# Kernel optimization log

Hardware: AMD Instinct MI355X
Metric: run time of the kernel (lower is better)

## Reference

```python
import jax, jax.numpy as jnp
import numpy as np

H = 16
N_TASKS, N_DATA, N_DEV = 400_000, 200_000, 8


def _edges(key, n_src, n_dst, e):
    k1, k2 = jax.random.split(key)
    src = jax.random.randint(k1, (e,), 0, n_src)
    dst = jax.random.randint(k2, (e,), 0, n_dst)
    return jnp.stack([src, dst]).astype(jnp.int64)


def setup_inputs() -> dict:
    key = jax.random.key(0)
    ks = jax.random.split(key, 16)
    inp = {
        "x_tasks": jax.random.normal(ks[0], (N_TASKS, 12), jnp.float32),
        "x_data": jax.random.normal(ks[1], (N_DATA, 5), jnp.float32),
        "x_devices": jax.random.normal(ks[2], (N_DEV, 12), jnp.float32),
        "ei_data_tasks": _edges(ks[3], N_DATA, N_TASKS, 1_600_000),
        "ei_tasks_data": _edges(ks[4], N_TASKS, N_DATA, 1_600_000),
        "ei_tasks_devices": _edges(ks[5], N_TASKS, N_DEV, 400_000),
        "ei_devices_tasks": _edges(ks[6], N_DEV, N_TASKS, 400_000),
        "ei_data_devices": _edges(ks[7], N_DATA, N_DEV, 200_000),
        "ei_devices_data": _edges(ks[8], N_DEV, N_DATA, 200_000),
        "ei_tt_to": _edges(ks[9], N_TASKS, N_TASKS, 800_000),
        "ei_tt_from": _edges(ks[10], N_TASKS, N_TASKS, 800_000),
        # stacked GraphConv weights, grouped by input dim
        # W_rel5:  [0]=data->tasks, [1]=data->devices
        "W_rel5": jax.random.normal(ks[11], (2, 5, H), jnp.float32) * 0.3,
        # W_rel12: [0]=tasks->data,[1]=tasks->devices,[2]=devices->tasks,[3]=devices->data,[4]=tt_to,[5]=tt_from
        "W_rel12": jax.random.normal(ks[12], (6, 12, H), jnp.float32) * 0.2,
        # b_rel order: dt_t, t_d, t_dev, dev_t, d_dev, dev_d, tt_to, tt_from
        "b_rel": jax.random.normal(ks[13], (8, H), jnp.float32) * 0.1,
        # W_root5: [0]=tasks->data (dst data), [1]=devices->data
        "W_root5": jax.random.normal(ks[14], (2, 5, H), jnp.float32) * 0.3,
        # W_root12: [0]=data->tasks,[1]=tasks->devices,[2]=devices->tasks,[3]=data->devices,[4]=tt_to,[5]=tt_from
        "W_root12": jax.random.normal(ks[15], (6, 12, H), jnp.float32) * 0.2,
        # LayerNorm params: [0]=tasks, [1]=data, [2]=devices
        "ln_gamma": jnp.ones((3, H), jnp.float32),
        "ln_beta": jnp.zeros((3, H), jnp.float32),
    }
    return inp


def _graph_conv(x_src, x_dst, ei, W_rel, b_rel, W_root):
    # PyG GraphConv(aggr='add'): lin_rel(scatter_add(x_src[src] -> dst)) + lin_root(x_dst)
    agg = jax.ops.segment_sum(x_src[ei[0]], ei[1], num_segments=x_dst.shape[0])
    return agg @ W_rel + b_rel + x_dst @ W_root


def _layer_norm(x, gamma, beta, eps=1e-5):
    mu = jnp.mean(x, axis=-1, keepdims=True)
    var = jnp.mean(jnp.square(x - mu), axis=-1, keepdims=True)
    return (x - mu) * jax.lax.rsqrt(var + eps) * gamma + beta


def reference(x_tasks, x_data, x_devices,
              ei_data_tasks, ei_tasks_data, ei_tasks_devices, ei_devices_tasks,
              ei_data_devices, ei_devices_data, ei_tt_to, ei_tt_from,
              W_rel5, W_rel12, b_rel, W_root5, W_root12, ln_gamma, ln_beta):
    # HeteroConv(aggr='sum'): sum relation outputs per destination node type
    tasks = (
        _graph_conv(x_data, x_tasks, ei_data_tasks, W_rel5[0], b_rel[0], W_root12[0])
        + _graph_conv(x_devices, x_tasks, ei_devices_tasks, W_rel12[2], b_rel[3], W_root12[2])
        + _graph_conv(x_tasks, x_tasks, ei_tt_to, W_rel12[4], b_rel[6], W_root12[4])
        + _graph_conv(x_tasks, x_tasks, ei_tt_from, W_rel12[5], b_rel[7], W_root12[5])
    )
    data = (
        _graph_conv(x_tasks, x_data, ei_tasks_data, W_rel12[0], b_rel[1], W_root5[0])
        + _graph_conv(x_devices, x_data, ei_devices_data, W_rel12[3], b_rel[5], W_root5[1])
    )
    devices = (
        _graph_conv(x_tasks, x_devices, ei_tasks_devices, W_rel12[1], b_rel[2], W_root12[1])
        + _graph_conv(x_data, x_devices, ei_data_devices, W_rel5[1], b_rel[4], W_root12[3])
    )
    slope = 0.01
    tasks = jax.nn.leaky_relu(_layer_norm(tasks, ln_gamma[0], ln_beta[0]), slope)
    data = jax.nn.leaky_relu(_layer_norm(data, ln_gamma[1], ln_beta[1]), slope)
    devices = jax.nn.leaky_relu(_layer_norm(devices, ln_gamma[2], ln_beta[2]), slope)
    return tasks, data, devices
```

## Files before the change

kernel.cpp:

```cpp
#include <hip/hip_runtime.h>

#define LRELU(v) ((v) >= 0.0f ? (v) : 0.01f * (v))
#define EPB 8192
#define SHIFT_T 7
#define SHIFT_D 8
#define MAXB 3200

struct PartDesc {
    const int* src; const int* dst;
    unsigned int* part; int* cursor;
    int E, B, cap, shift, chunk0;
};
struct PartArgs { PartDesc r[6]; };

__global__ __launch_bounds__(256)
void partition_all_k(PartArgs a)
{
    __shared__ int hist[MAXB];
    __shared__ int base[MAXB];
    const int bid = blockIdx.x;
    int ri = 0;
    #pragma unroll
    for (int k = 1; k < 6; ++k) if (bid >= a.r[k].chunk0) ri = k;
    const PartDesc d = a.r[ri];
    const int t = threadIdx.x;
    const int e0 = (bid - d.chunk0) * EPB;
    const int e1 = min(d.E, e0 + EPB);
    const int B = d.B, sh = d.shift;
    const unsigned mask = (1u << sh) - 1u;

    for (int i = t; i < B; i += 256) hist[i] = 0;
    __syncthreads();
    for (int e = e0 + t; e < e1; e += 256)
        atomicAdd(&hist[d.dst[e] >> sh], 1);
    __syncthreads();
    for (int i = t; i < B; i += 256) {
        int h = hist[i];
        base[i] = h ? atomicAdd(&d.cursor[i], h) : 0;
        hist[i] = 0;
    }
    __syncthreads();
    for (int e = e0 + t; e < e1; e += 256) {
        int dd = d.dst[e];
        int b = dd >> sh;
        int r = atomicAdd(&hist[b], 1) + base[b];
        if (r < d.cap)
            d.part[(size_t)b * d.cap + r] =
                ((unsigned)d.src[e] << sh) | ((unsigned)dd & mask);
    }
}

template<int F>
__device__ __forceinline__ void loadrow(const float* __restrict__ x, unsigned s, float* v) {
    const float* p = x + (size_t)s * F;
    #pragma unroll
    for (int f = 0; f < F; ++f) v[f] = p[f];
}
template<>
__device__ __forceinline__ void loadrow<12>(const float* __restrict__ x, unsigned s, float* v) {
    const float4* p = (const float4*)(x + (size_t)s * 12);
    float4 a = p[0], b = p[1], c = p[2];
    v[0]=a.x; v[1]=a.y; v[2]=a.z; v[3]=a.w;
    v[4]=b.x; v[5]=b.y; v[6]=b.z; v[7]=b.w;
    v[8]=c.x; v[9]=c.y; v[10]=c.z; v[11]=c.w;
}
template<int F>
__device__ __forceinline__ void addrow(float* a, const float* v) {
    #pragma unroll
    for (int f = 0; f < F; ++f) atomicAdd(a + f, v[f]);
}

template<int F, int STRIDE, int BASE, int SHIFT>
__device__ __forceinline__
void agg_rel(const unsigned* __restrict__ p, int cnt, const float* __restrict__ x,
             float* acc, int t)
{
    constexpr unsigned MASK = (1u << SHIFT) - 1u;
    int i = 2 * t;
    for (; i + 1 < cnt; i += 512) {
        uint2 e = *(const uint2*)(p + i);
        float v0[F], v1[F];
        loadrow<F>(x, e.x >> SHIFT, v0);
        loadrow<F>(x, e.y >> SHIFT, v1);
        addrow<F>(acc + (e.x & MASK) * STRIDE + BASE, v0);
        addrow<F>(acc + (e.y & MASK) * STRIDE + BASE, v1);
    }
    if (i < cnt) {
        unsigned e = p[i];
        float v[F];
        loadrow<F>(x, e >> SHIFT, v);
        addrow<F>(acc + (e & MASK) * STRIDE + BASE, v);
    }
}

template<int NF>
__device__ __forceinline__
void dot_ln_store(const float* __restrict__ f, const float* __restrict__ sW,
                  const float* __restrict__ sb, const float* __restrict__ sg,
                  const float* __restrict__ sbt, float* __restrict__ op)
{
    float o[16];
    #pragma unroll
    for (int k = 0; k < 16; ++k) o[k] = sb[k];
    const float4* w4 = (const float4*)sW;
    #pragma unroll
    for (int j = 0; j < NF; ++j) {
        const float fj = f[j];
        float4 w0 = w4[j*4+0], w1 = w4[j*4+1], w2 = w4[j*4+2], w3 = w4[j*4+3];
        o[0] =fmaf(fj,w0.x,o[0]);  o[1] =fmaf(fj,w0.y,o[1]);
        o[2] =fmaf(fj,w0.z,o[2]);  o[3] =fmaf(fj,w0.w,o[3]);
        o[4] =fmaf(fj,w1.x,o[4]);  o[5] =fmaf(fj,w1.y,o[5]);
        o[6] =fmaf(fj,w1.z,o[6]);  o[7] =fmaf(fj,w1.w,o[7]);
        o[8] =fmaf(fj,w2.x,o[8]);  o[9] =fmaf(fj,w2.y,o[9]);
        o[10]=fmaf(fj,w2.z,o[10]); o[11]=fmaf(fj,w2.w,o[11]);
        o[12]=fmaf(fj,w3.x,o[12]); o[13]=fmaf(fj,w3.y,o[13]);
        o[14]=fmaf(fj,w3.z,o[14]); o[15]=fmaf(fj,w3.w,o[15]);
    }
    float mu = 0.0f;
    #pragma unroll
    for (int k = 0; k < 16; ++k) mu += o[k];
    mu *= 0.0625f;
    float var = 0.0f;
    #pragma unroll
    for (int k = 0; k < 16; ++k) { float d = o[k] - mu; var = fmaf(d, d, var); }
    var *= 0.0625f;
    const float r = rsqrtf(var + 1e-5f);
    #pragma unroll
    for (int k = 0; k < 16; ++k) {
        float v = (o[k] - mu) * r * sg[k] + sbt[k];
        op[k] = LRELU(v);
    }
}

struct FinArgs {
    const unsigned *p_dt, *p_devt, *p_to, *p_from, *p_td, *p_devd;
    const int *c_dt, *c_devt, *c_to, *c_from, *c_td, *c_devd;
    int cap_dt, cap_devt, cap_to, cap_from, cap_td, cap_devd;
    const float *x_tasks, *x_data, *x_dev;
    const float *W_rel5, *W_rel12, *b_rel, *W_root5, *W_root12, *ln_g, *ln_b;
    float *out_tasks, *out_data;
    int NT, ND, Bt;
};

__global__ __launch_bounds__(256, 4)
void agg_finalize_k(FinArgs A)
{
    __shared__ __align__(16) float lds[6912];
    const int t = threadIdx.x;

    if ((int)blockIdx.x < A.Bt) {
        float* sW  = lds;
        float* sb  = lds + 848;
        float* sg  = lds + 864;
        float* sbt = lds + 880;
        float* acc = lds + 896;
        const int b  = blockIdx.x;
        const int n0 = b << SHIFT_T;
        const int nn = min(128, A.NT - n0);
        for (int i = t; i < 80; i += 256) sW[i] = A.W_rel5[i];
        for (int i = t; i < 192; i += 256) {
            sW[80  + i] = A.W_rel12[384 + i];
            sW[272 + i] = A.W_rel12[768 + i];
            sW[464 + i] = A.W_rel12[960 + i];
            sW[656 + i] = A.W_root12[i] + A.W_root12[384 + i]
                        + A.W_root12[768 + i] + A.W_root12[960 + i];
        }
        if (t < 16) {
            sb[t]  = A.b_rel[t] + A.b_rel[48 + t] + A.b_rel[96 + t] + A.b_rel[112 + t];
            sg[t]  = A.ln_g[t];
            sbt[t] = A.ln_b[t];
        }
        for (int i = t; i < 128 * 41; i += 256) acc[i] = 0.0f;
        __syncthreads();

        agg_rel<5, 41, 0, SHIFT_T>(A.p_dt   + (size_t)b * A.cap_dt,   min(A.c_dt[b],   A.cap_dt),   A.x_data,  acc, t);
        agg_rel<12,41, 5, SHIFT_T>(A.p_devt + (size_t)b * A.cap_devt, min(A.c_devt[b], A.cap_devt), A.x_dev,   acc, t);
        agg_rel<12,41,17, SHIFT_T>(A.p_to   + (size_t)b * A.cap_to,   min(A.c_to[b],   A.cap_to),   A.x_tasks, acc, t);
        agg_rel<12,41,29, SHIFT_T>(A.p_from + (size_t)b * A.cap_from, min(A.c_from[b], A.cap_from), A.x_tasks, acc, t);
        __syncthreads();

        if (t < nn) {
            float f[53];
            #pragma unroll
            for (int j = 0; j < 41; ++j) f[j] = acc[t * 41 + j];
            const float* xr = A.x_tasks + (size_t)(n0 + t) * 12;
            #pragma unroll
            for (int j = 0; j < 12; ++j) f[41 + j] = xr[j];
            dot_ln_store<53>(f, sW, sb, sg, sbt, A.out_tasks + (size_t)(n0 + t) * 16);
        }
    } else {
        float* sW  = lds;
        float* sb  = lds + 464;
        float* sg  = lds + 480;
        float* sbt = lds + 496;
        float* acc = lds + 512;
        const int b  = blockIdx.x - A.Bt;
        const int n0 = b << SHIFT_D;
        const int nn = min(256, A.ND - n0);
        for (int i = t; i < 192; i += 256) {
            sW[i]       = A.W_rel12[i];
            sW[192 + i] = A.W_rel12[576 + i];
        }
        for (int i = t; i < 80; i += 256)
            sW[384 + i] = A.W_root5[i] + A.W_root5[80 + i];
        if (t < 16) {
            sb[t]  = A.b_rel[16 + t] + A.b_rel[80 + t];
            sg[t]  = A.ln_g[16 + t];
            sbt[t] = A.ln_b[16 + t];
        }
        for (int i = t; i < 256 * 25; i += 256) acc[i] = 0.0f;
        __syncthreads();

        agg_rel<12,25, 0, SHIFT_D>(A.p_td   + (size_t)b * A.cap_td,   min(A.c_td[b],   A.cap_td),   A.x_tasks, acc, t);
        agg_rel<12,25,12, SHIFT_D>(A.p_devd + (size_t)b * A.cap_devd, min(A.c_devd[b], A.cap_devd), A.x_dev,   acc, t);
        __syncthreads();

        if (t < nn) {
            float f[29];
            #pragma unroll
            for (int j = 0; j < 24; ++j) f[j] = acc[t * 25 + j];
            const float* xr = A.x_data + (size_t)(n0 + t) * 5;
            #pragma unroll
            for (int j = 0; j < 5; ++j) f[24 + j] = xr[j];
            dot_ln_store<29>(f, sW, sb, sg, sbt, A.out_data + (size_t)(n0 + t) * 16);
        }
    }
}

template<int F>
__global__ __launch_bounds__(256)
void scatter_dev_k(const float* __restrict__ x, const int* __restrict__ src,
                   const int* __restrict__ dst, int E, float* __restrict__ agg)
{
    __shared__ float s_agg[8 * F];
    for (int i = threadIdx.x; i < 8 * F; i += 256) s_agg[i] = 0.0f;
    __syncthreads();

    float acc[8 * F];
    #pragma unroll
    for (int i = 0; i < 8 * F; ++i) acc[i] = 0.0f;

    const int stride = gridDim.x * blockDim.x;
    for (int e = blockIdx.x * blockDim.x + threadIdx.x; e < E; e += stride) {
        int s = src[e];
        int d = dst[e];
        float xr[F];
        loadrow<F>(x, (unsigned)s, xr);
        #pragma unroll
        for (int dd = 0; dd < 8; ++dd) {
            bool m = (d == dd);
            #pragma unroll
            for (int f = 0; f < F; ++f)
                acc[dd * F + f] += m ? xr[f] : 0.0f;
        }
    }

    const int lane = threadIdx.x & 63;
    #pragma unroll
    for (int i = 0; i < 8 * F; ++i) {
        float v = acc[i];
        #pragma unroll
        for (int off = 32; off; off >>= 1) v += __shfl_down(v, off);
        if (lane == 0) atomicAdd(&s_agg[i], v);
    }
    __syncthreads();
    if (threadIdx.x < 8 * F) atomicAdd(&agg[threadIdx.x], s_agg[threadIdx.x]);
}

__global__ void finalize_dev_k(const float* __restrict__ aggT, const float* __restrict__ aggD,
                               const float* __restrict__ x,
                               const float* __restrict__ W_rel12, const float* __restrict__ W_rel5,
                               const float* __restrict__ b_rel, const float* __restrict__ W_root12,
                               const float* __restrict__ ln_g, const float* __restrict__ ln_b,
                               float* __restrict__ out, int N)
{
    int i = threadIdx.x;
    if (i >= N) return;
    float acc[16];
    #pragma unroll
    for (int k = 0; k < 16; ++k) acc[k] = b_rel[32 + k] + b_rel[64 + k];
    #pragma unroll
    for (int j = 0; j < 12; ++j) {
        float fj = aggT[i * 12 + j];
        #pragma unroll
        for (int k = 0; k < 16; ++k) acc[k] = fmaf(fj, W_rel12[192 + j * 16 + k], acc[k]);
    }
    #pragma unroll
    for (int j = 0; j < 5; ++j) {
        float fj = aggD[i * 5 + j];
        #pragma unroll
        for (int k = 0; k < 16; ++k) acc[k] = fmaf(fj, W_rel5[80 + j * 16 + k], acc[k]);
    }
    #pragma unroll
    for (int j = 0; j < 12; ++j) {
        float fj = x[i * 12 + j];
        #pragma unroll
        for (int k = 0; k < 16; ++k)
            acc[k] = fmaf(fj, W_root12[192 + j * 16 + k] + W_root12[576 + j * 16 + k], acc[k]);
    }
    float mu = 0.0f;
    #pragma unroll
    for (int k = 0; k < 16; ++k) mu += acc[k];
    mu *= 0.0625f;
    float var = 0.0f;
    #pragma unroll
    for (int k = 0; k < 16; ++k) { float d = acc[k] - mu; var = fmaf(d, d, var); }
    var *= 0.0625f;
    const float r = rsqrtf(var + 1e-5f);
    #pragma unroll
    for (int k = 0; k < 16; ++k) {
        float v = (acc[k] - mu) * r * ln_g[32 + k] + ln_b[32 + k];
        out[i * 16 + k] = LRELU(v);
    }
}

extern "C" void kernel_launch(void* const* d_in, const int* in_sizes, int n_in,
                              void* d_out, int out_size, void* d_ws, size_t ws_size,
                              hipStream_t stream)
{
    const float* x_tasks = (const float*)d_in[0];
    const float* x_data  = (const float*)d_in[1];
    const float* x_dev   = (const float*)d_in[2];
    const int* ei_dt    = (const int*)d_in[3];
    const int* ei_td    = (const int*)d_in[4];
    const int* ei_tdev  = (const int*)d_in[5];
    const int* ei_devt  = (const int*)d_in[6];
    const int* ei_ddev  = (const int*)d_in[7];
    const int* ei_devd  = (const int*)d_in[8];
    const int* ei_to    = (const int*)d_in[9];
    const int* ei_from  = (const int*)d_in[10];
    const float* W_rel5   = (const float*)d_in[11];
    const float* W_rel12  = (const float*)d_in[12];
    const float* b_rel    = (const float*)d_in[13];
    const float* W_root5  = (const float*)d_in[14];
    const float* W_root12 = (const float*)d_in[15];
    const float* ln_g     = (const float*)d_in[16];
    const float* ln_b     = (const float*)d_in[17];

    const int NT   = in_sizes[0] / 12;
    const int ND   = in_sizes[1] / 5;
    const int NDEV = in_sizes[2] / 12;
    const int E_dt   = in_sizes[3]  / 2;
    const int E_td   = in_sizes[4]  / 2;
    const int E_tdev = in_sizes[5]  / 2;
    const int E_devt = in_sizes[6]  / 2;
    const int E_ddev = in_sizes[7]  / 2;
    const int E_devd = in_sizes[8]  / 2;
    const int E_to   = in_sizes[9]  / 2;
    const int E_from = in_sizes[10] / 2;

    const int B_t = (NT + 127) / 128;
    const int B_d = (ND + 255) / 256;

    auto capf = [](int E, int B) {
        int mean = E / B + 1;
        int c = mean + 256 + mean / 8;
        return (c + 1) & ~1;
    };
    const int cap_dt   = capf(E_dt,   B_t);
    const int cap_devt = capf(E_devt, B_t);
    const int cap_to   = capf(E_to,   B_t);
    const int cap_from = capf(E_from, B_t);
    const int cap_td   = capf(E_td,   B_d);
    const int cap_devd = capf(E_devd, B_d);

    float* ws = (float*)d_ws;
    size_t o = 0;
    int* c_dt   = (int*)(ws + o); o += MAXB;
    int* c_devt = (int*)(ws + o); o += MAXB;
    int* c_to   = (int*)(ws + o); o += MAXB;
    int* c_from = (int*)(ws + o); o += MAXB;
    int* c_td   = (int*)(ws + o); o += 800;
    int* c_devd = (int*)(ws + o); o += 800;
    float* aggT_dev = ws + o; o += 96;
    float* aggD_dev = ws + o; o += 48;
    const size_t zero_bytes = o * sizeof(float);
    o = (o + 1) & ~(size_t)1;
    unsigned* p_dt   = (unsigned*)(ws + o); o += (size_t)B_t * cap_dt;
    unsigned* p_devt = (unsigned*)(ws + o); o += (size_t)B_t * cap_devt;
    unsigned* p_to   = (unsigned*)(ws + o); o += (size_t)B_t * cap_to;
    unsigned* p_from = (unsigned*)(ws + o); o += (size_t)B_t * cap_from;
    unsigned* p_td   = (unsigned*)(ws + o); o += (size_t)B_d * cap_td;
    unsigned* p_devd = (unsigned*)(ws + o); o += (size_t)B_d * cap_devd;

    hipMemsetAsync(d_ws, 0, zero_bytes, stream);

    auto nc = [](int e) { return (e + EPB - 1) / EPB; };
    PartArgs pa;
    int ch = 0;
    pa.r[0] = { ei_dt,   ei_dt   + E_dt,   p_dt,   c_dt,   E_dt,   B_t, cap_dt,   SHIFT_T, ch }; ch += nc(E_dt);
    pa.r[1] = { ei_devt, ei_devt + E_devt, p_devt, c_devt, E_devt, B_t, cap_devt, SHIFT_T, ch }; ch += nc(E_devt);
    pa.r[2] = { ei_to,   ei_to   + E_to,   p_to,   c_to,   E_to,   B_t, cap_to,   SHIFT_T, ch }; ch += nc(E_to);
    pa.r[3] = { ei_from, ei_from + E_from, p_from, c_from, E_from, B_t, cap_from, SHIFT_T, ch }; ch += nc(E_from);
    pa.r[4] = { ei_td,   ei_td   + E_td,   p_td,   c_td,   E_td,   B_d, cap_td,   SHIFT_D, ch }; ch += nc(E_td);
    pa.r[5] = { ei_devd, ei_devd + E_devd, p_devd, c_devd, E_devd, B_d, cap_devd, SHIFT_D, ch }; ch += nc(E_devd);

    partition_all_k<<<ch, 256, 0, stream>>>(pa);

    scatter_dev_k<12><<<256, 256, 0, stream>>>(x_tasks, ei_tdev, ei_tdev + E_tdev, E_tdev, aggT_dev);
    scatter_dev_k<5> <<<128, 256, 0, stream>>>(x_data,  ei_ddev, ei_ddev + E_ddev, E_ddev, aggD_dev);

    float* out_tasks = (float*)d_out;
    float* out_data  = out_tasks + (size_t)NT * 16;
    float* out_dev   = out_data  + (size_t)ND * 16;

    FinArgs fa;
    fa.p_dt = p_dt; fa.p_devt = p_devt; fa.p_to = p_to; fa.p_from = p_from;
    fa.p_td = p_td; fa.p_devd = p_devd;
    fa.c_dt = c_dt; fa.c_devt = c_devt; fa.c_to = c_to; fa.c_from = c_from;
    fa.c_td = c_td; fa.c_devd = c_devd;
    fa.cap_dt = cap_dt; fa.cap_devt = cap_devt; fa.cap_to = cap_to;
    fa.cap_from = cap_from; fa.cap_td = cap_td; fa.cap_devd = cap_devd;
    fa.x_tasks = x_tasks; fa.x_data = x_data; fa.x_dev = x_dev;
    fa.W_rel5 = W_rel5; fa.W_rel12 = W_rel12; fa.b_rel = b_rel;
    fa.W_root5 = W_root5; fa.W_root12 = W_root12; fa.ln_g = ln_g; fa.ln_b = ln_b;
    fa.out_tasks = out_tasks; fa.out_data = out_data;
    fa.NT = NT; fa.ND = ND; fa.Bt = B_t;

    agg_finalize_k<<<B_t + B_d, 256, 0, stream>>>(fa);

    finalize_dev_k<<<1, 64, 0, stream>>>(
        aggT_dev, aggD_dev, x_dev,
        W_rel12, W_rel5, b_rel, W_root12, ln_g, ln_b, out_dev, NDEV);
}
```

Before: 646.9 us.

## Gather node features from fp16 copies and merge prep kernels into one launch

Adds fp16 padded copies of task and data features, built inside a single merged prep kernel that also runs the edge partitioning and the device-destination scatters. The aggregation now gathers source rows from these half-precision copies, 32 bytes per task row instead of 48, and processes four edges per thread per iteration to expose more memory-level parallelism. The device scatter switches from per-thread masked register accumulation to shared-memory atomics. Intent is to cut gather bandwidth and launch count, at the cost of an extra conversion pass and reduced input precision in the aggregates.

```diff
diff --git a/kernel.cpp b/kernel.cpp
--- a/kernel.cpp
+++ b/kernel.cpp
@@ -1,4 +1,5 @@
 #include <hip/hip_runtime.h>
+#include <hip/hip_fp16.h>
 
 #define LRELU(v) ((v) >= 0.0f ? (v) : 0.01f * (v))
 #define EPB 8192
@@ -11,44 +12,17 @@
     unsigned int* part; int* cursor;
     int E, B, cap, shift, chunk0;
 };
-struct PartArgs { PartDesc r[6]; };
-
-__global__ __launch_bounds__(256)
-void partition_all_k(PartArgs a)
-{
-    __shared__ int hist[MAXB];
-    __shared__ int base[MAXB];
-    const int bid = blockIdx.x;
-    int ri = 0;
-    #pragma unroll
-    for (int k = 1; k < 6; ++k) if (bid >= a.r[k].chunk0) ri = k;
-    const PartDesc d = a.r[ri];
-    const int t = threadIdx.x;
-    const int e0 = (bid - d.chunk0) * EPB;
-    const int e1 = min(d.E, e0 + EPB);
-    const int B = d.B, sh = d.shift;
-    const unsigned mask = (1u << sh) - 1u;
-
-    for (int i = t; i < B; i += 256) hist[i] = 0;
-    __syncthreads();
-    for (int e = e0 + t; e < e1; e += 256)
-        atomicAdd(&hist[d.dst[e] >> sh], 1);
-    __syncthreads();
-    for (int i = t; i < B; i += 256) {
-        int h = hist[i];
-        base[i] = h ? atomicAdd(&d.cursor[i], h) : 0;
-        hist[i] = 0;
-    }
-    __syncthreads();
-    for (int e = e0 + t; e < e1; e += 256) {
-        int dd = d.dst[e];
-        int b = dd >> sh;
-        int r = atomicAdd(&hist[b], 1) + base[b];
-        if (r < d.cap)
-            d.part[(size_t)b * d.cap + r] =
-                ((unsigned)d.src[e] << sh) | ((unsigned)dd & mask);
-    }
-}
+
+struct PrepArgs {
+    PartDesc r[6];
+    int part_end;
+    const int *tdev_e; int E_tdev; int sd12_b0, sd12_nb;
+    const int *ddev_e; int E_ddev; int sd5_b0, sd5_nb;
+    const float *x_tasks, *x_data, *x_dev;
+    float *aggT_dev, *aggD_dev;
+    __half *h_tasks; int NT; int ct_b0;
+    __half *h_data;  int ND; int cd_b0;
+};
 
 template<int F>
 __device__ __forceinline__ void loadrow(const float* __restrict__ x, unsigned s, float* v) {
@@ -64,31 +38,161 @@
     v[4]=b.x; v[5]=b.y; v[6]=b.z; v[7]=b.w;
     v[8]=c.x; v[9]=c.y; v[10]=c.z; v[11]=c.w;
 }
+
+template<int F>
+__device__ void scatter_dev_body(const float* __restrict__ x, const int* __restrict__ src,
+                                 const int* __restrict__ dst, int E,
+                                 float* __restrict__ agg, float* s_agg,
+                                 int bl, int nb, int t)
+{
+    for (int i = t; i < 8 * F; i += 256) s_agg[i] = 0.0f;
+    __syncthreads();
+    const int stride = nb * 256;
+    for (int e = bl * 256 + t; e < E; e += stride) {
+        float v[F];
+        loadrow<F>(x, (unsigned)src[e], v);
+        int d = dst[e];
+        #pragma unroll
+        for (int f = 0; f < F; ++f) atomicAdd(&s_agg[d * F + f], v[f]);
+    }
+    __syncthreads();
+    if (t < 8 * F) atomicAdd(&agg[t], s_agg[t]);
+}
+
+__global__ __launch_bounds__(256)
+void prep_k(PrepArgs A)
+{
+    __shared__ int shmem[2 * MAXB];
+    const int bid = blockIdx.x;
+    const int t = threadIdx.x;
+
+    if (bid < A.part_end) {
+        int* hist = shmem;
+        int* base = shmem + MAXB;
+        int ri = 0;
+        #pragma unroll
+        for (int k = 1; k < 6; ++k) if (bid >= A.r[k].chunk0) ri = k;
+        const PartDesc d = A.r[ri];
+        const int e0 = (bid - d.chunk0) * EPB;
+        const int e1 = min(d.E, e0 + EPB);
+        const int B = d.B, sh = d.shift;
+        const unsigned mask = (1u << sh) - 1u;
+
+        for (int i = t; i < B; i += 256) hist[i] = 0;
+        __syncthreads();
+        for (int e = e0 + t; e < e1; e += 256)
+            atomicAdd(&hist[d.dst[e] >> sh], 1);
+        __syncthreads();
+        for (int i = t; i < B; i += 256) {
+            int h = hist[i];
+            base[i] = h ? atomicAdd(&d.cursor[i], h) : 0;
+            hist[i] = 0;
+        }
+        __syncthreads();
+        for (int e = e0 + t; e < e1; e += 256) {
+            int dd = d.dst[e];
+            int b = dd >> sh;
+            int r = atomicAdd(&hist[b], 1) + base[b];
+            if (r < d.cap)
+                d.part[(size_t)b * d.cap + r] =
+                    ((unsigned)d.src[e] << sh) | ((unsigned)dd & mask);
+        }
+    } else if (bid < A.sd5_b0) {
+        scatter_dev_body<12>(A.x_tasks, A.tdev_e, A.tdev_e + A.E_tdev, A.E_tdev,
+                             A.aggT_dev, (float*)shmem, bid - A.sd12_b0, A.sd12_nb, t);
+    } else if (bid < A.ct_b0) {
+        scatter_dev_body<5>(A.x_data, A.ddev_e, A.ddev_e + A.E_ddev, A.E_ddev,
+                            A.aggD_dev, (float*)shmem, bid - A.sd5_b0, A.sd5_nb, t);
+    } else if (bid < A.cd_b0) {
+        int row = (bid - A.ct_b0) * 256 + t;
+        if (row < A.NT) {
+            const float* xr = A.x_tasks + (size_t)row * 12;
+            __half h[16];
+            #pragma unroll
+            for (int j = 0; j < 12; ++j) h[j] = __float2half(xr[j]);
+            #pragma unroll
+            for (int j = 12; j < 16; ++j) h[j] = __half(0.0f);
+            uint4* dst = (uint4*)(A.h_tasks + (size_t)row * 16);
+            dst[0] = *(const uint4*)h;
+            dst[1] = *(const uint4*)(h + 8);
+        }
+    } else {
+        int row = (bid - A.cd_b0) * 256 + t;
+        if (row < A.ND) {
+            const float* xr = A.x_data + (size_t)row * 5;
+            __half h[8];
+            #pragma unroll
+            for (int j = 0; j < 5; ++j) h[j] = __float2half(xr[j]);
+            #pragma unroll
+            for (int j = 5; j < 8; ++j) h[j] = __half(0.0f);
+            *(uint4*)(A.h_data + (size_t)row * 8) = *(const uint4*)h;
+        }
+    }
+}
+
+struct LoadH8 {
+    const __half* x;
+    __device__ __forceinline__ void operator()(unsigned s, float* v) const {
+        uint4 u = *(const uint4*)(x + (size_t)s * 8);
+        const __half2* h = (const __half2*)&u;
+        float2 f0 = __half22float2(h[0]);
+        float2 f1 = __half22float2(h[1]);
+        float2 f2 = __half22float2(h[2]);
+        v[0] = f0.x; v[1] = f0.y; v[2] = f1.x; v[3] = f1.y; v[4] = f2.x;
+    }
+};
+struct LoadH16 {
+    const __half* x;
+    __device__ __forceinline__ void operator()(unsigned s, float* v) const {
+        const uint4* p = (const uint4*)(x + (size_t)s * 16);
+        uint4 u0 = p[0], u1 = p[1];
+        const __half2* a = (const __half2*)&u0;
+        const __half2* b = (const __half2*)&u1;
+        float2 f;
+        f = __half22float2(a[0]); v[0] = f.x; v[1] = f.y;
+        f = __half22float2(a[1]); v[2] = f.x; v[3] = f.y;
+        f = __half22float2(a[2]); v[4] = f.x; v[5] = f.y;
+        f = __half22float2(a[3]); v[6] = f.x; v[7] = f.y;
+        f = __half22float2(b[0]); v[8] = f.x; v[9] = f.y;
+        f = __half22float2(b[1]); v[10] = f.x; v[11] = f.y;
+    }
+};
+struct LoadF12 {
+    const float* x;
+    __device__ __forceinline__ void operator()(unsigned s, float* v) const {
+        loadrow<12>(x, s, v);
+    }
+};
+
 template<int F>
 __device__ __forceinline__ void addrow(float* a, const float* v) {
     #pragma unroll
     for (int f = 0; f < F; ++f) atomicAdd(a + f, v[f]);
 }
 
-template<int F, int STRIDE, int BASE, int SHIFT>
+template<int F, int STRIDE, int BASE, int SHIFT, class LD>
 __device__ __forceinline__
-void agg_rel(const unsigned* __restrict__ p, int cnt, const float* __restrict__ x,
-             float* acc, int t)
+void agg_rel4(const unsigned* __restrict__ p, int cnt, LD ld, float* acc, int t)
 {
     constexpr unsigned MASK = (1u << SHIFT) - 1u;
-    int i = 2 * t;
-    for (; i + 1 < cnt; i += 512) {
-        uint2 e = *(const uint2*)(p + i);
-        float v0[F], v1[F];
-        loadrow<F>(x, e.x >> SHIFT, v0);
-        loadrow<F>(x, e.y >> SHIFT, v1);
+    int i = 4 * t;
+    for (; i + 3 < cnt; i += 1024) {
+        uint4 e = *(const uint4*)(p + i);
+        float v0[F], v1[F], v2[F], v3[F];
+        ld(e.x >> SHIFT, v0);
+        ld(e.y >> SHIFT, v1);
+        ld(e.z >> SHIFT, v2);
+        ld(e.w >> SHIFT, v3);
         addrow<F>(acc + (e.x & MASK) * STRIDE + BASE, v0);
         addrow<F>(acc + (e.y & MASK) * STRIDE + BASE, v1);
-    }
-    if (i < cnt) {
-        unsigned e = p[i];
+        addrow<F>(acc + (e.z & MASK) * STRIDE + BASE, v2);
+        addrow<F>(acc + (e.w & MASK) * STRIDE + BASE, v3);
+    }
+    const int jend = min(i + 4, cnt);
+    for (int j = i; j < jend; ++j) {
+        unsigned e = p[j];
         float v[F];
-        loadrow<F>(x, e >> SHIFT, v);
+        ld(e >> SHIFT, v);
         addrow<F>(acc + (e & MASK) * STRIDE + BASE, v);
     }
 }
@@ -137,6 +241,7 @@
     const int *c_dt, *c_devt, *c_to, *c_from, *c_td, *c_devd;
     int cap_dt, cap_devt, cap_to, cap_from, cap_td, cap_devd;
     const float *x_tasks, *x_data, *x_dev;
+    const __half *h_tasks, *h_data;
     const float *W_rel5, *W_rel12, *b_rel, *W_root5, *W_root12, *ln_g, *ln_b;
     float *out_tasks, *out_data;
     int NT, ND, Bt;
@@ -173,10 +278,10 @@
         for (int i = t; i < 128 * 41; i += 256) acc[i] = 0.0f;
         __syncthreads();
 
-        agg_rel<5, 41, 0, SHIFT_T>(A.p_dt   + (size_t)b * A.cap_dt,   min(A.c_dt[b],   A.cap_dt),   A.x_data,  acc, t);
-        agg_rel<12,41, 5, SHIFT_T>(A.p_devt + (size_t)b * A.cap_devt, min(A.c_devt[b], A.cap_devt), A.x_dev,   acc, t);
-        agg_rel<12,41,17, SHIFT_T>(A.p_to   + (size_t)b * A.cap_to,   min(A.c_to[b],   A.cap_to),   A.x_tasks, acc, t);
-        agg_rel<12,41,29, SHIFT_T>(A.p_from + (size_t)b * A.cap_from, min(A.c_from[b], A.cap_from), A.x_tasks, acc, t);
+        agg_rel4<5, 41, 0, SHIFT_T>(A.p_dt   + (size_t)b * A.cap_dt,   min(A.c_dt[b],   A.cap_dt),   LoadH8{A.h_data},   acc, t);
+        agg_rel4<12,41, 5, SHIFT_T>(A.p_devt + (size_t)b * A.cap_devt, min(A.c_devt[b], A.cap_devt), LoadF12{A.x_dev},   acc, t);
+        agg_rel4<12,41,17, SHIFT_T>(A.p_to   + (size_t)b * A.cap_to,   min(A.c_to[b],   A.cap_to),   LoadH16{A.h_tasks}, acc, t);
+        agg_rel4<12,41,29, SHIFT_T>(A.p_from + (size_t)b * A.cap_from, min(A.c_from[b], A.cap_from), LoadH16{A.h_tasks}, acc, t);
         __syncthreads();
 
         if (t < nn) {
@@ -211,8 +316,8 @@
         for (int i = t; i < 256 * 25; i += 256) acc[i] = 0.0f;
         __syncthreads();
 
-        agg_rel<12,25, 0, SHIFT_D>(A.p_td   + (size_t)b * A.cap_td,   min(A.c_td[b],   A.cap_td),   A.x_tasks, acc, t);
-        agg_rel<12,25,12, SHIFT_D>(A.p_devd + (size_t)b * A.cap_devd, min(A.c_devd[b], A.cap_devd), A.x_dev,   acc, t);
+        agg_rel4<12,25, 0, SHIFT_D>(A.p_td   + (size_t)b * A.cap_td,   min(A.c_td[b],   A.cap_td),   LoadH16{A.h_tasks}, acc, t);
+        agg_rel4<12,25,12, SHIFT_D>(A.p_devd + (size_t)b * A.cap_devd, min(A.c_devd[b], A.cap_devd), LoadF12{A.x_dev},   acc, t);
         __syncthreads();
 
         if (t < nn) {
@@ -225,46 +330,6 @@
             dot_ln_store<29>(f, sW, sb, sg, sbt, A.out_data + (size_t)(n0 + t) * 16);
         }
     }
-}
-
-template<int F>
-__global__ __launch_bounds__(256)
-void scatter_dev_k(const float* __restrict__ x, const int* __restrict__ src,
-                   const int* __restrict__ dst, int E, float* __restrict__ agg)
-{
-    __shared__ float s_agg[8 * F];
-    for (int i = threadIdx.x; i < 8 * F; i += 256) s_agg[i] = 0.0f;
-    __syncthreads();
-
-    float acc[8 * F];
-    #pragma unroll
-    for (int i = 0; i < 8 * F; ++i) acc[i] = 0.0f;
-
-    const int stride = gridDim.x * blockDim.x;
-    for (int e = blockIdx.x * blockDim.x + threadIdx.x; e < E; e += stride) {
-        int s = src[e];
-        int d = dst[e];
-        float xr[F];
-        loadrow<F>(x, (unsigned)s, xr);
-        #pragma unroll
-        for (int dd = 0; dd < 8; ++dd) {
-            bool m = (d == dd);
-            #pragma unroll
-            for (int f = 0; f < F; ++f)
-                acc[dd * F + f] += m ? xr[f] : 0.0f;
-        }
-    }
-
-    const int lane = threadIdx.x & 63;
-    #pragma unroll
-    for (int i = 0; i < 8 * F; ++i) {
-        float v = acc[i];
-        #pragma unroll
-        for (int off = 32; off; off >>= 1) v += __shfl_down(v, off);
-        if (lane == 0) atomicAdd(&s_agg[i], v);
-    }
-    __syncthreads();
-    if (threadIdx.x < 8 * F) atomicAdd(&agg[threadIdx.x], s_agg[threadIdx.x]);
 }
 
 __global__ void finalize_dev_k(const float* __restrict__ aggT, const float* __restrict__ aggD,
@@ -355,7 +420,7 @@
     auto capf = [](int E, int B) {
         int mean = E / B + 1;
         int c = mean + 256 + mean / 8;
-        return (c + 1) & ~1;
+        return (c + 3) & ~3;
     };
     const int cap_dt   = capf(E_dt,   B_t);
     const int cap_devt = capf(E_devt, B_t);
@@ -375,7 +440,9 @@
     float* aggT_dev = ws + o; o += 96;
     float* aggD_dev = ws + o; o += 48;
     const size_t zero_bytes = o * sizeof(float);
-    o = (o + 1) & ~(size_t)1;
+    o = (o + 3) & ~(size_t)3;
+    __half* h_tasks = (__half*)(ws + o); o += (size_t)NT * 8;
+    __half* h_data  = (__half*)(ws + o); o += (size_t)ND * 4;
     unsigned* p_dt   = (unsigned*)(ws + o); o += (size_t)B_t * cap_dt;
     unsigned* p_devt = (unsigned*)(ws + o); o += (size_t)B_t * cap_devt;
     unsigned* p_to   = (unsigned*)(ws + o); o += (size_t)B_t * cap_to;
@@ -386,7 +453,7 @@
     hipMemsetAsync(d_ws, 0, zero_bytes, stream);
 
     auto nc = [](int e) { return (e + EPB - 1) / EPB; };
-    PartArgs pa;
+    PrepArgs pa;
     int ch = 0;
     pa.r[0] = { ei_dt,   ei_dt   + E_dt,   p_dt,   c_dt,   E_dt,   B_t, cap_dt,   SHIFT_T, ch }; ch += nc(E_dt);
     pa.r[1] = { ei_devt, ei_devt + E_devt, p_devt, c_devt, E_devt, B_t, cap_devt, SHIFT_T, ch }; ch += nc(E_devt);
@@ -394,11 +461,15 @@
     pa.r[3] = { ei_from, ei_from + E_from, p_from, c_from, E_from, B_t, cap_from, SHIFT_T, ch }; ch += nc(E_from);
     pa.r[4] = { ei_td,   ei_td   + E_td,   p_td,   c_td,   E_td,   B_d, cap_td,   SHIFT_D, ch }; ch += nc(E_td);
     pa.r[5] = { ei_devd, ei_devd + E_devd, p_devd, c_devd, E_devd, B_d, cap_devd, SHIFT_D, ch }; ch += nc(E_devd);
-
-    partition_all_k<<<ch, 256, 0, stream>>>(pa);
-
-    scatter_dev_k<12><<<256, 256, 0, stream>>>(x_tasks, ei_tdev, ei_tdev + E_tdev, E_tdev, aggT_dev);
-    scatter_dev_k<5> <<<128, 256, 0, stream>>>(x_data,  ei_ddev, ei_ddev + E_ddev, E_ddev, aggD_dev);
+    pa.part_end = ch;
+    pa.tdev_e = ei_tdev; pa.E_tdev = E_tdev; pa.sd12_b0 = ch; pa.sd12_nb = 192; ch += 192;
+    pa.ddev_e = ei_ddev; pa.E_ddev = E_ddev; pa.sd5_b0  = ch; pa.sd5_nb  = 96;  ch += 96;
+    pa.x_tasks = x_tasks; pa.x_data = x_data; pa.x_dev = x_dev;
+    pa.aggT_dev = aggT_dev; pa.aggD_dev = aggD_dev;
+    pa.h_tasks = h_tasks; pa.NT = NT; pa.ct_b0 = ch; ch += (NT + 255) / 256;
+    pa.h_data  = h_data;  pa.ND = ND; pa.cd_b0 = ch; ch += (ND + 255) / 256;
+
+    prep_k<<<ch, 256, 0, stream>>>(pa);
 
     float* out_tasks = (float*)d_out;
     float* out_data  = out_tasks + (size_t)NT * 16;
@@ -412,6 +483,7 @@
     fa.cap_dt = cap_dt; fa.cap_devt = cap_devt; fa.cap_to = cap_to;
     fa.cap_from = cap_from; fa.cap_td = cap_td; fa.cap_devd = cap_devd;
     fa.x_tasks = x_tasks; fa.x_data = x_data; fa.x_dev = x_dev;
+    fa.h_tasks = h_tasks; fa.h_data = h_data;
     fa.W_rel5 = W_rel5; fa.W_rel12 = W_rel12; fa.b_rel = b_rel;
     fa.W_root5 = W_root5; fa.W_root12 = W_root12; fa.ln_g = ln_g; fa.ln_b = ln_b;
     fa.out_tasks = out_tasks; fa.out_data = out_data;
```

New measurement: 637.4 us. No clear change (-1.5%).
